# Performance work log

Hardware: AMD Instinct MI355X
Metric: run time of the kernel (lower is better)

The kernel has to match this reference:

```python
import jax, jax.numpy as jnp
import numpy as np

N = 100000   # nodes
E = 3200000  # edges
D = 256      # hidden_dim
G = 512      # graphs in batch
NEG_SLOPE = 0.2


def segment_softmax(logits, seg, num_segments):
    # numerically stable per-segment softmax over dim 0
    m = jax.ops.segment_max(logits, seg, num_segments=num_segments)
    m = jnp.where(jnp.isfinite(m), m, 0.0)  # empty segments -> 0
    e = jnp.exp(logits - m[seg])
    s = jax.ops.segment_sum(e, seg, num_segments=num_segments)
    return e / (s[seg] + 1e-16)


def setup_inputs() -> dict:
    key = jax.random.key(0)
    ks = jax.random.split(key, 6)
    x = jax.random.normal(ks[0], (N, D), dtype=jnp.float32)
    edge_index = jax.random.randint(ks[1], (2, E), 0, N, dtype=jnp.int32)
    batch = jnp.sort(jax.random.randint(ks[2], (N,), 0, G, dtype=jnp.int32))
    # GATConv(hidden_dim, 1) params (heads=1): lin weight, att vectors, bias
    W = jax.random.normal(ks[3], (D, 1), dtype=jnp.float32) / np.sqrt(D).astype(np.float32)
    att_src = jax.random.normal(ks[4], (1,), dtype=jnp.float32)
    att_dst = jax.random.normal(ks[5], (1,), dtype=jnp.float32)
    bias = jnp.zeros((1,), dtype=jnp.float32)
    return {"x": x, "edge_index": edge_index, "batch": batch,
            "W": W, "att_src": att_src, "att_dst": att_dst, "bias": bias}


def reference(x, edge_index, batch, W, att_src, att_dst, bias):
    n = x.shape[0]
    # --- GATConv(hidden_dim, 1), heads=1, add_self_loops=True ---
    h = x @ W                               # [N,1]
    a_s = (h * att_src).squeeze(-1)         # [N]
    a_d = (h * att_dst).squeeze(-1)         # [N]
    loops = jnp.arange(n, dtype=edge_index.dtype)
    src = jnp.concatenate([edge_index[0], loops])   # [E+N]
    dst = jnp.concatenate([edge_index[1], loops])   # [E+N]
    e = jax.nn.leaky_relu(a_s[src] + a_d[dst], NEG_SLOPE)
    alpha = segment_softmax(e, dst, n)               # softmax over incoming edges
    x_conv = jax.ops.segment_sum(alpha[:, None] * h[src], dst, num_segments=n) + bias  # [N,1]
    # --- segment softmax over graphs, then scatter-add pooling ---
    scores = segment_softmax(x_conv.squeeze(-1), batch, G)[:, None]  # [N,1]
    gx = jax.ops.segment_sum(x * scores, batch, num_segments=G)       # [G,D]
    return gx
```

## Files before the change

kernel.cpp:

```cpp
#include <hip/hip_runtime.h>
#include <stdint.h>

#define NEG_SLOPE 0.2f
#define DHID 256
#define BSZ_SHIFT 10
#define BSZ (1 << BSZ_SHIFT)
#define MAXNB 128
#define PSUB 16
#define SCHUNK 4096
#define KSUB 4

__device__ __forceinline__ float lrelu(float e) {
    return (e >= 0.0f) ? e : NEG_SLOPE * e;
}
__device__ __forceinline__ float dot4(float4 a, float4 b) {
    return a.x * b.x + a.y * b.y + a.z * b.z + a.w * b.w;
}

__global__ __launch_bounds__(256) void k1_h_bounds(
    const float* __restrict__ x, const float* __restrict__ W,
    float* __restrict__ h, int N,
    const int* __restrict__ batch, int* __restrict__ start, int G,
    float* __restrict__ gsum, int* __restrict__ cursor, int NB,
    int nRowBlk, int nBndBlk)
{
    if (blockIdx.x >= (unsigned)nRowBlk) {
        int rb = blockIdx.x - nRowBlk;
        if (rb == nBndBlk) {
            for (int t = threadIdx.x; t < G; t += 256) gsum[t] = 0.0f;
            for (int t = threadIdx.x; t < NB; t += 256) cursor[t] = 0;
            return;
        }
        int i = rb * 256 + threadIdx.x;
        if (i >= N) return;
        int b = batch[i];
        if (i == 0) {
            for (int g = 0; g <= b; ++g) start[g] = 0;
        } else {
            int bp = batch[i - 1];
            for (int g = bp + 1; g <= b; ++g) start[g] = i;
        }
        if (i == N - 1) {
            for (int g = b + 1; g <= G; ++g) start[g] = N;
        }
        return;
    }

    int wave = threadIdx.x >> 6;
    int lane = threadIdx.x & 63;
    int r = lane >> 4;
    int c = lane & 15;
    int row = blockIdx.x * 16 + wave * 4 + r;
    if (row >= N) return;

    float4 wv0 = *(const float4*)(W + c * 4);
    float4 wv1 = *(const float4*)(W + 64 + c * 4);
    float4 wv2 = *(const float4*)(W + 128 + c * 4);
    float4 wv3 = *(const float4*)(W + 192 + c * 4);
    const float* xr = x + (size_t)row * DHID;
    float4 a0 = *(const float4*)(xr + c * 4);
    float4 a1 = *(const float4*)(xr + 64 + c * 4);
    float4 a2 = *(const float4*)(xr + 128 + c * 4);
    float4 a3 = *(const float4*)(xr + 192 + c * 4);
    float s = dot4(a0, wv0) + dot4(a1, wv1) + dot4(a2, wv2) + dot4(a3, wv3);
    s += __shfl_xor(s, 1);
    s += __shfl_xor(s, 2);
    s += __shfl_xor(s, 4);
    s += __shfl_xor(s, 8);
    if (c == 0) h[row] = s;
}

__global__ __launch_bounds__(512) void k_scatter(
    const int* __restrict__ src, const int* __restrict__ dst, int E, int NB,
    int* __restrict__ cursor, uint32_t* __restrict__ pairs, int CAP)
{
    __shared__ int cnt[MAXNB];
    __shared__ int loff[MAXNB];
    __shared__ int base_g[MAXNB];
    __shared__ int lcur[MAXNB];
    __shared__ uint32_t buf[SCHUNK];
    __shared__ uint8_t binOf[SCHUNK];

    int e0 = blockIdx.x * SCHUNK;
    int e1 = min(e0 + SCHUNK, E);
    int nch = e1 - e0;
    int t = threadIdx.x;

    int sv[8], dv[8];
#pragma unroll
    for (int k = 0; k < 8; ++k) {
        int e = e0 + k * 512 + t;
        if (e < e1) { sv[k] = src[e]; dv[k] = dst[e]; }
    }

    for (int q = t; q < MAXNB; q += 512) { cnt[q] = 0; lcur[q] = 0; }
    __syncthreads();
#pragma unroll
    for (int k = 0; k < 8; ++k) {
        int e = e0 + k * 512 + t;
        if (e < e1) atomicAdd(&cnt[dv[k] >> BSZ_SHIFT], 1);
    }
    __syncthreads();
    if (t < 64) {
        int v0 = cnt[t], v1 = cnt[64 + t];
        int s0 = v0, s1 = v1;
#pragma unroll
        for (int d = 1; d < 64; d <<= 1) {
            int u0 = __shfl_up(s0, d);
            int u1 = __shfl_up(s1, d);
            if (t >= d) { s0 += u0; s1 += u1; }
        }
        int tot0 = __shfl(s0, 63);
        loff[t]      = s0 - v0;
        loff[64 + t] = s1 + tot0 - v1;
    }
    __syncthreads();
    for (int q = t; q < MAXNB; q += 512)
        if (q < NB && cnt[q] > 0) base_g[q] = atomicAdd(&cursor[q], cnt[q]);
    __syncthreads();
#pragma unroll
    for (int k = 0; k < 8; ++k) {
        int e = e0 + k * 512 + t;
        if (e < e1) {
            int d = dv[k];
            int bin = d >> BSZ_SHIFT;
            int r = atomicAdd(&lcur[bin], 1);
            int q = loff[bin] + r;
            buf[q] = ((uint32_t)sv[k] << BSZ_SHIFT) | (uint32_t)(d & (BSZ - 1));
            binOf[q] = (uint8_t)bin;
        }
    }
    __syncthreads();
    for (int q = t; q < nch; q += 512) {
        int b = binOf[q];
        pairs[(size_t)b * CAP + base_g[b] + (q - loff[b])] = buf[q];
    }
}

__global__ __launch_bounds__(256) void k_accum(
    const uint32_t* __restrict__ pairs, const int* __restrict__ cursor,
    const float* __restrict__ h,
    const float* __restrict__ att_src, const float* __restrict__ att_dst,
    float* __restrict__ partials, int N, int CAP)
{
    __shared__ float dacc[BSZ];
    __shared__ float nacc[BSZ];
    __shared__ float hbuf[BSZ];
    int b = blockIdx.x / PSUB;
    int s = blockIdx.x % PSUB;
    int base = b << BSZ_SHIFT;

    for (int t = threadIdx.x; t < BSZ; t += 256) {
        dacc[t] = 0.0f; nacc[t] = 0.0f;
        int gi = base + t;
        hbuf[t] = (gi < N) ? h[gi] : 0.0f;
    }
    __syncthreads();

    int count = cursor[b];
    int per = (count + PSUB - 1) / PSUB;
    int i0 = s * per;
    int i1 = min(i0 + per, count);

    float as = att_src[0], ad = att_dst[0];
    const uint32_t* bp = pairs + (size_t)b * CAP;
    for (int i = i0 + threadIdx.x; i < i1; i += 256) {
        uint32_t pr = bp[i];
        int ld = (int)(pr & (BSZ - 1));
        float hs = h[pr >> BSZ_SHIFT];
        float w = __expf(lrelu(as * hs + ad * hbuf[ld]));
        atomicAdd(&dacc[ld], w);
        atomicAdd(&nacc[ld], w * hs);
    }
    __syncthreads();
    float* out = partials + ((size_t)blockIdx.x * 2) * BSZ;
    for (int t = threadIdx.x; t < BSZ; t += 256) {
        out[t]       = dacc[t];
        out[BSZ + t] = nacc[t];
    }
}

__global__ __launch_bounds__(256) void k3_scores_p(
    const float* __restrict__ partials, const float* __restrict__ h,
    const float* __restrict__ att_src, const float* __restrict__ att_dst,
    const float* __restrict__ bias, const int* __restrict__ batch,
    float* __restrict__ escore, float* __restrict__ gsum, int N)
{
    __shared__ float bins[64];
    __shared__ int bbase_s;
    int i = blockIdx.x * 256 + threadIdx.x;
    if (threadIdx.x == 0) {
        int i0 = blockIdx.x * 256;
        bbase_s = batch[i0 < N ? i0 : N - 1];
    }
    for (int t = threadIdx.x; t < 64; t += 256) bins[t] = 0.0f;

    float w = 0.0f;
    int b = -1;
    if (i < N) {
        int bk = i >> BSZ_SHIFT;
        int pos = i & (BSZ - 1);
        float dsum = 0.0f, nsum = 0.0f;
#pragma unroll
        for (int p = 0; p < PSUB; ++p) {
            const float* pp = partials + ((size_t)(bk * PSUB + p) * 2) * BSZ;
            dsum += pp[pos];
            nsum += pp[BSZ + pos];
        }
        float hi = h[i];
        float e0 = lrelu((att_src[0] + att_dst[0]) * hi);
        float ws = __expf(e0);
        dsum += ws;
        nsum += ws * hi;
        float xc = nsum / (dsum + 1e-16f) + bias[0];
        w = __expf(xc);
        escore[i] = w;
        b = batch[i];
    }
    __syncthreads();
    if (i < N) {
        int off = b - bbase_s;
        if (off >= 0 && off < 64) atomicAdd(&bins[off], w);
        else                      atomicAdd(&gsum[b], w);
    }
    __syncthreads();
    for (int t = threadIdx.x; t < 64; t += 256)
        if (bins[t] != 0.0f) atomicAdd(&gsum[bbase_s + t], bins[t]);
}

__global__ __launch_bounds__(256) void k4_pool(
    const float* __restrict__ x, const float* __restrict__ escore,
    const float* __restrict__ gsum, const int* __restrict__ start,
    float* __restrict__ gxp, int G)
{
    int g = blockIdx.x >> 2;
    int s = blockIdx.x & 3;
    int st = start[g], en = start[g + 1];
    float inv = 1.0f / (gsum[g] + 1e-16f);
    int tid    = threadIdx.x;
    int col4   = (tid & 63) << 2;
    int rowOff = tid >> 6;

    float4 acc = make_float4(0.f, 0.f, 0.f, 0.f);
    int i = st + s * 4 + rowOff;
    for (; i + 16 < en; i += 32) {
        float sc0 = escore[i] * inv;
        float sc1 = escore[i + 16] * inv;
        float4 v0 = *(const float4*)(x + (size_t)i * DHID + col4);
        float4 v1 = *(const float4*)(x + (size_t)(i + 16) * DHID + col4);
        acc.x += v0.x * sc0 + v1.x * sc1;
        acc.y += v0.y * sc0 + v1.y * sc1;
        acc.z += v0.z * sc0 + v1.z * sc1;
        acc.w += v0.w * sc0 + v1.w * sc1;
    }
    if (i < en) {
        float sc = escore[i] * inv;
        float4 v = *(const float4*)(x + (size_t)i * DHID + col4);
        acc.x += v.x * sc; acc.y += v.y * sc;
        acc.z += v.z * sc; acc.w += v.w * sc;
    }

    __shared__ float4 red[256];
    red[tid] = acc;
    __syncthreads();
    if (tid < 64) {
        float4 a = red[tid], b = red[tid + 64], c = red[tid + 128], d = red[tid + 192];
        float4 r;
        r.x = a.x + b.x + c.x + d.x;
        r.y = a.y + b.y + c.y + d.y;
        r.z = a.z + b.z + c.z + d.z;
        r.w = a.w + b.w + c.w + d.w;
        *(float4*)(gxp + ((size_t)s * G + g) * DHID + col4) = r;
    }
}

__global__ __launch_bounds__(256) void k5_merge(
    const float* __restrict__ gxp, float* __restrict__ gx, int total)
{
    int j = blockIdx.x * 256 + threadIdx.x;
    if (j < total)
        gx[j] = gxp[j] + gxp[total + j] + gxp[2 * total + j] + gxp[3 * total + j];
}

__global__ __launch_bounds__(256) void k0_zero_fb(float* __restrict__ p, int n) {
    int i = blockIdx.x * 256 + threadIdx.x;
    if (i < n) p[i] = 0.0f;
}
__global__ __launch_bounds__(256) void k2_edges_fb(
    const int* __restrict__ src, const int* __restrict__ dst,
    const float* __restrict__ h,
    const float* __restrict__ att_src, const float* __restrict__ att_dst,
    float* __restrict__ denom, float* __restrict__ num, int E)
{
    int i = blockIdx.x * 256 + threadIdx.x;
    if (i >= E) return;
    int s = src[i], d = dst[i];
    float as = att_src[0], ad = att_dst[0];
    float hs = h[s];
    float w = expf(lrelu(as * hs + ad * h[d]));
    atomicAdd(&denom[d], w);
    atomicAdd(&num[d],   w * hs);
}
__global__ __launch_bounds__(256) void k3_scores_fb(
    const float* __restrict__ denom, const float* __restrict__ num,
    const float* __restrict__ h,
    const float* __restrict__ att_src, const float* __restrict__ att_dst,
    const float* __restrict__ bias, const int* __restrict__ batch,
    float* __restrict__ escore, float* __restrict__ gsum, int N)
{
    __shared__ float bins[64];
    __shared__ int bbase_s;
    int i = blockIdx.x * 256 + threadIdx.x;
    if (threadIdx.x == 0) {
        int i0 = blockIdx.x * 256;
        bbase_s = batch[i0 < N ? i0 : N - 1];
    }
    for (int t = threadIdx.x; t < 64; t += 256) bins[t] = 0.0f;
    float w = 0.0f;
    int b = -1;
    if (i < N) {
        float hi = h[i];
        float ws = expf(lrelu((att_src[0] + att_dst[0]) * hi));
        float dsum = denom[i] + ws;
        float nsum = num[i] + ws * hi;
        float xc = nsum / (dsum + 1e-16f) + bias[0];
        w = expf(xc);
        escore[i] = w;
        b = batch[i];
    }
    __syncthreads();
    if (i < N) {
        int off = b - bbase_s;
        if (off >= 0 && off < 64) atomicAdd(&bins[off], w);
        else                      atomicAdd(&gsum[b], w);
    }
    __syncthreads();
    for (int t = threadIdx.x; t < 64; t += 256)
        if (bins[t] != 0.0f) atomicAdd(&gsum[bbase_s + t], bins[t]);
}

extern "C" void kernel_launch(void* const* d_in, const int* in_sizes, int n_in,
                              void* d_out, int out_size, void* d_ws, size_t ws_size,
                              hipStream_t stream) {
    const float* x        = (const float*)d_in[0];
    const int*   eidx     = (const int*)d_in[1];
    const int*   batch    = (const int*)d_in[2];
    const float* W        = (const float*)d_in[3];
    const float* att_src  = (const float*)d_in[4];
    const float* att_dst  = (const float*)d_in[5];
    const float* bias     = (const float*)d_in[6];
    float*       gx       = (float*)d_out;

    const int N = in_sizes[2];
    const int E = in_sizes[1] / 2;
    const int G = out_size / DHID;
    const int NB = (N + BSZ - 1) >> BSZ_SHIFT;
    const int CAP = ((E / NB + 8192) + 255) & ~255;

    const int* src = eidx;
    const int* dst = eidx + E;

    char* p = (char*)d_ws;
    auto alloc = [&](size_t bytes) {
        char* q = p;
        p += (bytes + 255) & ~(size_t)255;
        return q;
    };
    float* h      = (float*)alloc((size_t)N * 4);
    float* escore = (float*)alloc((size_t)N * 4);
    float* gsum   = (float*)alloc((size_t)G * 4);
    int*   startA = (int*)alloc((size_t)(G + 1) * 4);

    size_t fixed = (size_t)(p - (char*)d_ws);
    size_t need_full = fixed
        + 512 + (size_t)NB * 4
        + 512 + (size_t)NB * CAP * 4
        + 512 + (size_t)NB * PSUB * 2 * BSZ * 4
        + 512 + (size_t)KSUB * G * DHID * 4;

    bool full = (NB <= MAXNB) && (N <= (1 << (32 - BSZ_SHIFT)))
             && (need_full + 4096 <= ws_size);

    int nRowBlk = (N + 15) / 16;
    int nBndBlk = (N + 255) / 256;

    if (full) {
        int*      cursor   = (int*)alloc((size_t)NB * 4);
        uint32_t* pairs    = (uint32_t*)alloc((size_t)NB * CAP * 4);
        float*    partials = (float*)alloc((size_t)NB * PSUB * 2 * BSZ * 4);
        float*    gxp      = (float*)alloc((size_t)KSUB * G * DHID * 4);

        int sgrid = (E + SCHUNK - 1) / SCHUNK;

        k1_h_bounds<<<nRowBlk + nBndBlk + 1, 256, 0, stream>>>(
            x, W, h, N, batch, startA, G, gsum, cursor, NB, nRowBlk, nBndBlk);
        k_scatter<<<sgrid, 512, 0, stream>>>(src, dst, E, NB, cursor,
                                             pairs, CAP);
        k_accum<<<NB * PSUB, 256, 0, stream>>>(pairs, cursor, h,
                                               att_src, att_dst, partials,
                                               N, CAP);
        k3_scores_p<<<(N + 255) / 256, 256, 0, stream>>>(partials, h,
                                                         att_src, att_dst, bias,
                                                         batch, escore, gsum, N);
        k4_pool<<<G * KSUB, 256, 0, stream>>>(x, escore, gsum, startA, gxp, G);
        k5_merge<<<(G * DHID + 255) / 256, 256, 0, stream>>>(gxp, gx, G * DHID);
    } else {
        float* denom = (float*)alloc((size_t)N * 4);
        float* num   = (float*)alloc((size_t)N * 4);
        float* gxp   = (float*)alloc((size_t)KSUB * G * DHID * 4);
        int*   dummyCur = (int*)alloc(256);
        k0_zero_fb<<<(2 * N + 255) / 256, 256, 0, stream>>>(denom, 2 * N);
        k1_h_bounds<<<nRowBlk + nBndBlk + 1, 256, 0, stream>>>(
            x, W, h, N, batch, startA, G, gsum, dummyCur, 0, nRowBlk, nBndBlk);
        k2_edges_fb<<<(E + 255) / 256, 256, 0, stream>>>(src, dst, h,
                                                         att_src, att_dst,
                                                         denom, num, E);
        k3_scores_fb<<<(N + 255) / 256, 256, 0, stream>>>(denom, num, h,
                                                          att_src, att_dst, bias,
                                                          batch, escore, gsum, N);
        k4_pool<<<G * KSUB, 256, 0, stream>>>(x, escore, gsum, startA, gxp, G);
        k5_merge<<<(G * DHID + 255) / 256, 256, 0, stream>>>(gxp, gx, G * DHID);
    }
}
```

Measured before the change: 109.8 us.

## Reuse scatter ranks, vectorize edge accumulation, fuse pooling into single 1024-thread kernel

The scatter kernel now keeps the rank returned by the counting atomic, so the second round of shared-memory atomics used for placement is no longer needed. The accumulation kernel reads packed edge pairs four at a time with uint4 loads, and pads each sub-range to a multiple of four so those loads stay aligned. Pooling now runs as one 1024-thread block per graph that writes gx directly, which removes the partial buffer and the merge kernel launch. The trade-off is less parallelism in pooling (512 blocks instead of 2048) and a larger shared-memory reduction per block.

```diff
diff --git a/kernel.cpp b/kernel.cpp
--- a/kernel.cpp
+++ b/kernel.cpp
@@ -8,7 +8,6 @@
 #define MAXNB 128
 #define PSUB 16
 #define SCHUNK 4096
-#define KSUB 4
 
 __device__ __forceinline__ float lrelu(float e) {
     return (e >= 0.0f) ? e : NEG_SLOPE * e;
@@ -77,7 +76,6 @@
     __shared__ int cnt[MAXNB];
     __shared__ int loff[MAXNB];
     __shared__ int base_g[MAXNB];
-    __shared__ int lcur[MAXNB];
     __shared__ uint32_t buf[SCHUNK];
     __shared__ uint8_t binOf[SCHUNK];
 
@@ -86,19 +84,19 @@
     int nch = e1 - e0;
     int t = threadIdx.x;
 
-    int sv[8], dv[8];
+    int sv[8], dv[8], rk[8];
 #pragma unroll
     for (int k = 0; k < 8; ++k) {
         int e = e0 + k * 512 + t;
         if (e < e1) { sv[k] = src[e]; dv[k] = dst[e]; }
     }
 
-    for (int q = t; q < MAXNB; q += 512) { cnt[q] = 0; lcur[q] = 0; }
+    for (int q = t; q < MAXNB; q += 512) cnt[q] = 0;
     __syncthreads();
 #pragma unroll
     for (int k = 0; k < 8; ++k) {
         int e = e0 + k * 512 + t;
-        if (e < e1) atomicAdd(&cnt[dv[k] >> BSZ_SHIFT], 1);
+        if (e < e1) rk[k] = atomicAdd(&cnt[dv[k] >> BSZ_SHIFT], 1);
     }
     __syncthreads();
     if (t < 64) {
@@ -122,11 +120,10 @@
     for (int k = 0; k < 8; ++k) {
         int e = e0 + k * 512 + t;
         if (e < e1) {
-            int d = dv[k];
-            int bin = d >> BSZ_SHIFT;
-            int r = atomicAdd(&lcur[bin], 1);
-            int q = loff[bin] + r;
-            buf[q] = ((uint32_t)sv[k] << BSZ_SHIFT) | (uint32_t)(d & (BSZ - 1));
+            int bin = dv[k] >> BSZ_SHIFT;
+            int q = loff[bin] + rk[k];
+            buf[q] = ((uint32_t)sv[k] << BSZ_SHIFT) |
+                     (uint32_t)(dv[k] & (BSZ - 1));
             binOf[q] = (uint8_t)bin;
         }
     }
@@ -158,13 +155,34 @@
     __syncthreads();
 
     int count = cursor[b];
-    int per = (count + PSUB - 1) / PSUB;
+    int per = (((count + PSUB - 1) / PSUB) + 3) & ~3;
     int i0 = s * per;
     int i1 = min(i0 + per, count);
 
     float as = att_src[0], ad = att_dst[0];
     const uint32_t* bp = pairs + (size_t)b * CAP;
-    for (int i = i0 + threadIdx.x; i < i1; i += 256) {
+
+    int i = i0 + threadIdx.x * 4;
+    for (; i + 3 < i1; i += 1024) {
+        uint4 pr4 = *(const uint4*)(bp + i);
+        float hs0 = h[pr4.x >> BSZ_SHIFT];
+        float hs1 = h[pr4.y >> BSZ_SHIFT];
+        float hs2 = h[pr4.z >> BSZ_SHIFT];
+        float hs3 = h[pr4.w >> BSZ_SHIFT];
+        int l0 = (int)(pr4.x & (BSZ - 1));
+        int l1 = (int)(pr4.y & (BSZ - 1));
+        int l2 = (int)(pr4.z & (BSZ - 1));
+        int l3 = (int)(pr4.w & (BSZ - 1));
+        float w0 = __expf(lrelu(as * hs0 + ad * hbuf[l0]));
+        float w1 = __expf(lrelu(as * hs1 + ad * hbuf[l1]));
+        float w2 = __expf(lrelu(as * hs2 + ad * hbuf[l2]));
+        float w3 = __expf(lrelu(as * hs3 + ad * hbuf[l3]));
+        atomicAdd(&dacc[l0], w0); atomicAdd(&nacc[l0], w0 * hs0);
+        atomicAdd(&dacc[l1], w1); atomicAdd(&nacc[l1], w1 * hs1);
+        atomicAdd(&dacc[l2], w2); atomicAdd(&nacc[l2], w2 * hs2);
+        atomicAdd(&dacc[l3], w3); atomicAdd(&nacc[l3], w3 * hs3);
+    }
+    for (; i < i1; ++i) {
         uint32_t pr = bp[i];
         int ld = (int)(pr & (BSZ - 1));
         float hs = h[pr >> BSZ_SHIFT];
@@ -228,13 +246,13 @@
         if (bins[t] != 0.0f) atomicAdd(&gsum[bbase_s + t], bins[t]);
 }
 
-__global__ __launch_bounds__(256) void k4_pool(
+__global__ __launch_bounds__(1024) void k4_pool(
     const float* __restrict__ x, const float* __restrict__ escore,
     const float* __restrict__ gsum, const int* __restrict__ start,
-    float* __restrict__ gxp, int G)
-{
-    int g = blockIdx.x >> 2;
-    int s = blockIdx.x & 3;
+    float* __restrict__ gx)
+{
+    __shared__ float4 red[1024];
+    int g = blockIdx.x;
     int st = start[g], en = start[g + 1];
     float inv = 1.0f / (gsum[g] + 1e-16f);
     int tid    = threadIdx.x;
@@ -242,44 +260,24 @@
     int rowOff = tid >> 6;
 
     float4 acc = make_float4(0.f, 0.f, 0.f, 0.f);
-    int i = st + s * 4 + rowOff;
-    for (; i + 16 < en; i += 32) {
-        float sc0 = escore[i] * inv;
-        float sc1 = escore[i + 16] * inv;
-        float4 v0 = *(const float4*)(x + (size_t)i * DHID + col4);
-        float4 v1 = *(const float4*)(x + (size_t)(i + 16) * DHID + col4);
-        acc.x += v0.x * sc0 + v1.x * sc1;
-        acc.y += v0.y * sc0 + v1.y * sc1;
-        acc.z += v0.z * sc0 + v1.z * sc1;
-        acc.w += v0.w * sc0 + v1.w * sc1;
-    }
-    if (i < en) {
+    for (int i = st + rowOff; i < en; i += 16) {
         float sc = escore[i] * inv;
         float4 v = *(const float4*)(x + (size_t)i * DHID + col4);
         acc.x += v.x * sc; acc.y += v.y * sc;
         acc.z += v.z * sc; acc.w += v.w * sc;
     }
 
-    __shared__ float4 red[256];
     red[tid] = acc;
     __syncthreads();
     if (tid < 64) {
-        float4 a = red[tid], b = red[tid + 64], c = red[tid + 128], d = red[tid + 192];
-        float4 r;
-        r.x = a.x + b.x + c.x + d.x;
-        r.y = a.y + b.y + c.y + d.y;
-        r.z = a.z + b.z + c.z + d.z;
-        r.w = a.w + b.w + c.w + d.w;
-        *(float4*)(gxp + ((size_t)s * G + g) * DHID + col4) = r;
-    }
-}
-
-__global__ __launch_bounds__(256) void k5_merge(
-    const float* __restrict__ gxp, float* __restrict__ gx, int total)
-{
-    int j = blockIdx.x * 256 + threadIdx.x;
-    if (j < total)
-        gx[j] = gxp[j] + gxp[total + j] + gxp[2 * total + j] + gxp[3 * total + j];
+        float4 r = red[tid];
+#pragma unroll
+        for (int k = 1; k < 16; ++k) {
+            float4 v = red[tid + 64 * k];
+            r.x += v.x; r.y += v.y; r.z += v.z; r.w += v.w;
+        }
+        *(float4*)(gx + (size_t)g * DHID + col4) = r;
+    }
 }
 
 __global__ __launch_bounds__(256) void k0_zero_fb(float* __restrict__ p, int n) {
@@ -375,8 +373,7 @@
     size_t need_full = fixed
         + 512 + (size_t)NB * 4
         + 512 + (size_t)NB * CAP * 4
-        + 512 + (size_t)NB * PSUB * 2 * BSZ * 4
-        + 512 + (size_t)KSUB * G * DHID * 4;
+        + 512 + (size_t)NB * PSUB * 2 * BSZ * 4;
 
     bool full = (NB <= MAXNB) && (N <= (1 << (32 - BSZ_SHIFT)))
              && (need_full + 4096 <= ws_size);
@@ -388,7 +385,6 @@
         int*      cursor   = (int*)alloc((size_t)NB * 4);
         uint32_t* pairs    = (uint32_t*)alloc((size_t)NB * CAP * 4);
         float*    partials = (float*)alloc((size_t)NB * PSUB * 2 * BSZ * 4);
-        float*    gxp      = (float*)alloc((size_t)KSUB * G * DHID * 4);
 
         int sgrid = (E + SCHUNK - 1) / SCHUNK;
 
@@ -402,12 +398,10 @@
         k3_scores_p<<<(N + 255) / 256, 256, 0, stream>>>(partials, h,
                                                          att_src, att_dst, bias,
                                                          batch, escore, gsum, N);
-        k4_pool<<<G * KSUB, 256, 0, stream>>>(x, escore, gsum, startA, gxp, G);
-        k5_merge<<<(G * DHID + 255) / 256, 256, 0, stream>>>(gxp, gx, G * DHID);
+        k4_pool<<<G, 1024, 0, stream>>>(x, escore, gsum, startA, gx);
     } else {
         float* denom = (float*)alloc((size_t)N * 4);
         float* num   = (float*)alloc((size_t)N * 4);
-        float* gxp   = (float*)alloc((size_t)KSUB * G * DHID * 4);
         int*   dummyCur = (int*)alloc(256);
         k0_zero_fb<<<(2 * N + 255) / 256, 256, 0, stream>>>(denom, 2 * N);
         k1_h_bounds<<<nRowBlk + nBndBlk + 1, 256, 0, stream>>>(
@@ -418,7 +412,6 @@
         k3_scores_fb<<<(N + 255) / 256, 256, 0, stream>>>(denom, num, h,
                                                           att_src, att_dst, bias,
                                                           batch, escore, gsum, N);
-        k4_pool<<<G * KSUB, 256, 0, stream>>>(x, escore, gsum, startA, gxp, G);
-        k5_merge<<<(G * DHID + 255) / 256, 256, 0, stream>>>(gxp, gx, G * DHID);
-    }
-}
+        k4_pool<<<G, 1024, 0, stream>>>(x, escore, gsum, startA, gx);
+    }
+}
```

Result: faster. 107.1 us (-2.5%).
